# Performance work log

Hardware: AMD Instinct MI355X
Metric: run time of the kernel (lower is better)

## Reference

```python
import jax, jax.numpy as jnp
import numpy as np

N_NODES = 50000
N_EDGES = 800000
D_IN = 128
D_OUT = 128


def setup_inputs() -> dict:
    key = jax.random.key(0)
    ks = jax.random.split(key, 6)
    x = jax.random.normal(ks[0], (N_NODES, D_IN), dtype=jnp.float32)
    edge_src = jax.random.randint(ks[1], (N_EDGES,), 0, N_NODES)
    edge_dst = jax.random.randint(ks[2], (N_EDGES,), 0, N_NODES)
    edge_val = jax.random.uniform(ks[3], (N_EDGES,), dtype=jnp.float32)
    W = jax.random.normal(ks[4], (D_OUT, D_IN), dtype=jnp.float32) / np.sqrt(D_IN)
    b = jax.random.normal(ks[5], (D_OUT,), dtype=jnp.float32) * 0.01
    return {"x": x, "edge_src": edge_src, "edge_dst": edge_dst,
            "edge_val": edge_val, "W": W, "b": b}


def reference(x, edge_src, edge_dst, edge_val, W, b):
    # h = sparse.mm(adj, x): for each edge (dst, src, val): h[dst] += val * x[src]
    msgs = edge_val[:, None] * x[edge_src]            # [E, D_IN]
    h = jax.ops.segment_sum(msgs, edge_dst, num_segments=N_NODES)  # [N, D_IN]
    # nn.Linear: h @ W.T + b, then relu activation
    out = jnp.einsum('nd,od->no', h, W) + b           # [N, D_OUT]
    return jax.nn.relu(out)
```

## Files before the change

kernel.cpp:

```cpp
#include <hip/hip_runtime.h>
#include <hip/hip_bf16.h>

#define N_NODES 50000
#define N_EDGES 800000
#define D 128
#define CAP 64
#define EPT 8
#define BUCKET_NB 391
#define GEMM_NB 256
#define AGG_BPQ 782
#define YSLICE (N_NODES * 16)

static_assert(N_NODES < 65536, "src must fit in 16 bits for epack");
static_assert(BUCKET_NB * 256 * EPT >= N_EDGES, "bucket grid covers all edges");

typedef __attribute__((ext_vector_type(8))) short short8;
typedef __attribute__((ext_vector_type(4))) float f32x4;
typedef unsigned int uint;
typedef unsigned short ushort;

__device__ __forceinline__ ushort f2bf(float f) {
    uint u = __float_as_uint(f);
    u += 0x7fffu + ((u >> 16) & 1u);
    return (ushort)(u >> 16);
}

__device__ __forceinline__ float bflo(uint u) { return __uint_as_float(u << 16); }
__device__ __forceinline__ float bfhi(uint u) { return __uint_as_float(u & 0xffff0000u); }


__global__ __launch_bounds__(256) void sgcn_fat(
    const float* __restrict__ x, const float* __restrict__ W,
    const int* __restrict__ src, const int* __restrict__ dst,
    const float* __restrict__ val, int* __restrict__ deg,
    uint* __restrict__ epack, ushort* __restrict__ y)
{
    if (blockIdx.x < BUCKET_NB) {
        int t = blockIdx.x * 256 + threadIdx.x;
        const int T = BUCKET_NB * 256;
        int  d[EPT], s[EPT], r[EPT];
        float v[EPT];
        bool ok[EPT];
#pragma unroll
        for (int i = 0; i < EPT; ++i) {
            int e = t + i * T;
            ok[i] = e < N_EDGES;
            if (ok[i]) { d[i] = dst[e]; s[i] = src[e]; v[i] = val[e]; }
        }
#pragma unroll
        for (int i = 0; i < EPT; ++i)
            if (ok[i]) r[i] = atomicAdd(&deg[d[i]], 1);
#pragma unroll
        for (int i = 0; i < EPT; ++i)
            if (ok[i] && r[i] < CAP)
                epack[(size_t)d[i] * CAP + r[i]] = ((uint)f2bf(v[i]) << 16) | (uint)s[i];
        return;
    }

    int gb   = blockIdx.x - BUCKET_NB;
    int wave = threadIdx.x >> 6;
    int lane = threadIdx.x & 63;
    int lm = lane & 15;
    int kb = lane >> 4;

    short8 bfr[8][4];
#pragma unroll
    for (int nt = 0; nt < 8; ++nt)
#pragma unroll
        for (int kk = 0; kk < 4; ++kk) {
            const float* wp = W + (nt * 16 + lm) * D + kk * 32 + kb * 8;
            float4 a = *reinterpret_cast<const float4*>(wp);
            float4 c = *reinterpret_cast<const float4*>(wp + 4);
            short8 s;
            s[0] = (short)f2bf(a.x); s[1] = (short)f2bf(a.y);
            s[2] = (short)f2bf(a.z); s[3] = (short)f2bf(a.w);
            s[4] = (short)f2bf(c.x); s[5] = (short)f2bf(c.y);
            s[6] = (short)f2bf(c.z); s[7] = (short)f2bf(c.w);
            bfr[nt][kk] = s;
        }

    const int nMT = N_NODES / 16;
    int mt0 = gb * 4 + wave;
    const int strideMT = GEMM_NB * 4;
    for (int mt = mt0; mt < nMT; mt += strideMT) {
        int m0 = mt * 16;
        const float* xrow = x + (long)(m0 + lm) * D + kb * 8;
        short8 afr[4];
#pragma unroll
        for (int kk = 0; kk < 4; ++kk) {
            float4 a = *reinterpret_cast<const float4*>(xrow + kk * 32);
            float4 c = *reinterpret_cast<const float4*>(xrow + kk * 32 + 4);
            short8 s;
            s[0] = (short)f2bf(a.x); s[1] = (short)f2bf(a.y);
            s[2] = (short)f2bf(a.z); s[3] = (short)f2bf(a.w);
            s[4] = (short)f2bf(c.x); s[5] = (short)f2bf(c.y);
            s[6] = (short)f2bf(c.z); s[7] = (short)f2bf(c.w);
            afr[kk] = s;
        }
#pragma unroll
        for (int nt = 0; nt < 8; ++nt) {
            f32x4 acc = {0.f, 0.f, 0.f, 0.f};
#pragma unroll
            for (int kk = 0; kk < 4; ++kk)
                acc = __builtin_amdgcn_mfma_f32_16x16x32_bf16(afr[kk], bfr[nt][kk], acc, 0, 0, 0);
            int q = nt >> 1;
            ushort* yp = y + ((size_t)q * N_NODES + (m0 + kb * 4)) * 32 + (nt & 1) * 16 + lm;
#pragma unroll
            for (int r = 0; r < 4; ++r)
                yp[(size_t)r * 32] = f2bf(acc[r]);
        }
    }
}


__global__ __launch_bounds__(256) void sgcn_aggregate(
    const uint* __restrict__ yb, const int* __restrict__ deg,
    const uint* __restrict__ ep, const float* __restrict__ bias,
    float* __restrict__ out)
{
    int q  = blockIdx.x & 3;
    int nb = blockIdx.x >> 2;
    int n  = nb * 64 + (threadIdx.x >> 2);
    if (n >= N_NODES) return;
    int c4 = threadIdx.x & 3;
    int ch = q * 32 + c4 * 8;
    const uint* ys = yb + (size_t)q * YSLICE;

    float4 bv0 = *reinterpret_cast<const float4*>(bias + ch);
    float4 bv1 = *reinterpret_cast<const float4*>(bias + ch + 4);

    int dn = deg[n]; if (dn > CAP) dn = CAP;
    int j0 = n * CAP, j1 = j0 + dn;
    float a0 = 0.f, a1 = 0.f, a2 = 0.f, a3 = 0.f;
    float a4 = 0.f, a5 = 0.f, a6 = 0.f, a7 = 0.f;
    int j = j0;
    for (; j + 2 <= j1; j += 2) {
        uint p0 = ep[j];
        uint p1 = ep[j + 1];
        uint4 u0 = *reinterpret_cast<const uint4*>(ys + (size_t)(p0 & 0xffffu) * 16 + c4 * 4);
        uint4 u1 = *reinterpret_cast<const uint4*>(ys + (size_t)(p1 & 0xffffu) * 16 + c4 * 4);
        float v0 = __uint_as_float(p0 & 0xffff0000u);
        float v1 = __uint_as_float(p1 & 0xffff0000u);
        a0 += v0 * bflo(u0.x) + v1 * bflo(u1.x);
        a1 += v0 * bfhi(u0.x) + v1 * bfhi(u1.x);
        a2 += v0 * bflo(u0.y) + v1 * bflo(u1.y);
        a3 += v0 * bfhi(u0.y) + v1 * bfhi(u1.y);
        a4 += v0 * bflo(u0.z) + v1 * bflo(u1.z);
        a5 += v0 * bfhi(u0.z) + v1 * bfhi(u1.z);
        a6 += v0 * bflo(u0.w) + v1 * bflo(u1.w);
        a7 += v0 * bfhi(u0.w) + v1 * bfhi(u1.w);
    }
    if (j < j1) {
        uint p = ep[j];
        uint4 u = *reinterpret_cast<const uint4*>(ys + (size_t)(p & 0xffffu) * 16 + c4 * 4);
        float v = __uint_as_float(p & 0xffff0000u);
        a0 += v * bflo(u.x); a1 += v * bfhi(u.x);
        a2 += v * bflo(u.y); a3 += v * bfhi(u.y);
        a4 += v * bflo(u.z); a5 += v * bfhi(u.z);
        a6 += v * bflo(u.w); a7 += v * bfhi(u.w);
    }
    f32x4 r0, r1;
    r0[0] = fmaxf(a0 + bv0.x, 0.f);
    r0[1] = fmaxf(a1 + bv0.y, 0.f);
    r0[2] = fmaxf(a2 + bv0.z, 0.f);
    r0[3] = fmaxf(a3 + bv0.w, 0.f);
    r1[0] = fmaxf(a4 + bv1.x, 0.f);
    r1[1] = fmaxf(a5 + bv1.y, 0.f);
    r1[2] = fmaxf(a6 + bv1.z, 0.f);
    r1[3] = fmaxf(a7 + bv1.w, 0.f);
    f32x4* op = reinterpret_cast<f32x4*>(out + (long)n * D + ch);
    __builtin_nontemporal_store(r0, op);
    __builtin_nontemporal_store(r1, op + 1);
}

extern "C" void kernel_launch(void* const* d_in, const int* in_sizes, int n_in,
                              void* d_out, int out_size, void* d_ws, size_t ws_size,
                              hipStream_t stream) {
    const float* x   = (const float*)d_in[0];
    const int*   es  = (const int*)d_in[1];
    const int*   ed  = (const int*)d_in[2];
    const float* ev  = (const float*)d_in[3];
    const float* W   = (const float*)d_in[4];
    const float* b   = (const float*)d_in[5];
    float* out = (float*)d_out;

    char* ws = (char*)d_ws;
    size_t off = 0;
    uint* yb    = (uint*)(ws + off); off += (size_t)4 * YSLICE * sizeof(uint);
    uint* epack = (uint*)(ws + off); off += (size_t)N_NODES * CAP * sizeof(uint);
    int*  deg   = (int*) (ws + off); off += (size_t)N_NODES * sizeof(int);

    (void)hipMemsetAsync(deg, 0, (size_t)N_NODES * sizeof(int), stream);
    sgcn_fat<<<BUCKET_NB + GEMM_NB, 256, 0, stream>>>(x, W, es, ed, ev, deg, epack, (ushort*)yb);
    sgcn_aggregate<<<AGG_BPQ * 4, 256, 0, stream>>>(yb, deg, epack, b, out);
}
```

Measured before the change: 100.7 us.

## Split edge bucketing by destination half to overlap with aggregation

Bucketing is split into two passes by destination node range. The second-half bucketing runs in the same launch as aggregation of the first half, and a third kernel aggregates the second half. The aim is to hide atomic bucketing cost behind the GEMM and aggregation work. In exchange the edge dst array is read twice, the src/val loads become filtered, and there is one more kernel launch.

```diff
diff --git a/kernel.cpp b/kernel.cpp
--- a/kernel.cpp
+++ b/kernel.cpp
@@ -2,13 +2,14 @@
 #include <hip/hip_bf16.h>
 
 #define N_NODES 50000
+#define HALF 25000
 #define N_EDGES 800000
 #define D 128
 #define CAP 64
 #define EPT 8
 #define BUCKET_NB 391
 #define GEMM_NB 256
-#define AGG_BPQ 782
+#define AGG_HB 391
 #define YSLICE (N_NODES * 16)
 
 static_assert(N_NODES < 65536, "src must fit in 16 bits for epack");
@@ -29,99 +30,45 @@
 __device__ __forceinline__ float bfhi(uint u) { return __uint_as_float(u & 0xffff0000u); }
 
 
-__global__ __launch_bounds__(256) void sgcn_fat(
-    const float* __restrict__ x, const float* __restrict__ W,
-    const int* __restrict__ src, const int* __restrict__ dst,
+__device__ __forceinline__ void bucket_body(
+    int bid, const int* __restrict__ src, const int* __restrict__ dst,
     const float* __restrict__ val, int* __restrict__ deg,
-    uint* __restrict__ epack, ushort* __restrict__ y)
-{
-    if (blockIdx.x < BUCKET_NB) {
-        int t = blockIdx.x * 256 + threadIdx.x;
-        const int T = BUCKET_NB * 256;
-        int  d[EPT], s[EPT], r[EPT];
-        float v[EPT];
-        bool ok[EPT];
-#pragma unroll
-        for (int i = 0; i < EPT; ++i) {
-            int e = t + i * T;
-            ok[i] = e < N_EDGES;
-            if (ok[i]) { d[i] = dst[e]; s[i] = src[e]; v[i] = val[e]; }
-        }
-#pragma unroll
-        for (int i = 0; i < EPT; ++i)
-            if (ok[i]) r[i] = atomicAdd(&deg[d[i]], 1);
-#pragma unroll
-        for (int i = 0; i < EPT; ++i)
-            if (ok[i] && r[i] < CAP)
-                epack[(size_t)d[i] * CAP + r[i]] = ((uint)f2bf(v[i]) << 16) | (uint)s[i];
-        return;
-    }
-
-    int gb   = blockIdx.x - BUCKET_NB;
-    int wave = threadIdx.x >> 6;
-    int lane = threadIdx.x & 63;
-    int lm = lane & 15;
-    int kb = lane >> 4;
-
-    short8 bfr[8][4];
-#pragma unroll
-    for (int nt = 0; nt < 8; ++nt)
-#pragma unroll
-        for (int kk = 0; kk < 4; ++kk) {
-            const float* wp = W + (nt * 16 + lm) * D + kk * 32 + kb * 8;
-            float4 a = *reinterpret_cast<const float4*>(wp);
-            float4 c = *reinterpret_cast<const float4*>(wp + 4);
-            short8 s;
-            s[0] = (short)f2bf(a.x); s[1] = (short)f2bf(a.y);
-            s[2] = (short)f2bf(a.z); s[3] = (short)f2bf(a.w);
-            s[4] = (short)f2bf(c.x); s[5] = (short)f2bf(c.y);
-            s[6] = (short)f2bf(c.z); s[7] = (short)f2bf(c.w);
-            bfr[nt][kk] = s;
-        }
-
-    const int nMT = N_NODES / 16;
-    int mt0 = gb * 4 + wave;
-    const int strideMT = GEMM_NB * 4;
-    for (int mt = mt0; mt < nMT; mt += strideMT) {
-        int m0 = mt * 16;
-        const float* xrow = x + (long)(m0 + lm) * D + kb * 8;
-        short8 afr[4];
-#pragma unroll
-        for (int kk = 0; kk < 4; ++kk) {
-            float4 a = *reinterpret_cast<const float4*>(xrow + kk * 32);
-            float4 c = *reinterpret_cast<const float4*>(xrow + kk * 32 + 4);
-            short8 s;
-            s[0] = (short)f2bf(a.x); s[1] = (short)f2bf(a.y);
-            s[2] = (short)f2bf(a.z); s[3] = (short)f2bf(a.w);
-            s[4] = (short)f2bf(c.x); s[5] = (short)f2bf(c.y);
-            s[6] = (short)f2bf(c.z); s[7] = (short)f2bf(c.w);
-            afr[kk] = s;
-        }
-#pragma unroll
-        for (int nt = 0; nt < 8; ++nt) {
-            f32x4 acc = {0.f, 0.f, 0.f, 0.f};
-#pragma unroll
-            for (int kk = 0; kk < 4; ++kk)
-                acc = __builtin_amdgcn_mfma_f32_16x16x32_bf16(afr[kk], bfr[nt][kk], acc, 0, 0, 0);
-            int q = nt >> 1;
-            ushort* yp = y + ((size_t)q * N_NODES + (m0 + kb * 4)) * 32 + (nt & 1) * 16 + lm;
-#pragma unroll
-            for (int r = 0; r < 4; ++r)
-                yp[(size_t)r * 32] = f2bf(acc[r]);
-        }
-    }
-}
-
-
-__global__ __launch_bounds__(256) void sgcn_aggregate(
-    const uint* __restrict__ yb, const int* __restrict__ deg,
+    uint* __restrict__ epack, int dlo, int dhi)
+{
+    int t = bid * 256 + threadIdx.x;
+    const int T = BUCKET_NB * 256;
+    int  d[EPT], s[EPT], r[EPT];
+    float v[EPT];
+    bool ok[EPT];
+#pragma unroll
+    for (int i = 0; i < EPT; ++i) {
+        int e = t + i * T;
+        ok[i] = false;
+        if (e < N_EDGES) {
+            d[i] = dst[e];
+            ok[i] = (d[i] >= dlo) && (d[i] < dhi);
+            if (ok[i]) { s[i] = src[e]; v[i] = val[e]; }
+        }
+    }
+#pragma unroll
+    for (int i = 0; i < EPT; ++i)
+        if (ok[i]) r[i] = atomicAdd(&deg[d[i]], 1);
+#pragma unroll
+    for (int i = 0; i < EPT; ++i)
+        if (ok[i] && r[i] < CAP)
+            epack[(size_t)d[i] * CAP + r[i]] = ((uint)f2bf(v[i]) << 16) | (uint)s[i];
+}
+
+__device__ __forceinline__ void agg_body(
+    int bid, int nbase, const uint* __restrict__ yb, const int* __restrict__ deg,
     const uint* __restrict__ ep, const float* __restrict__ bias,
     float* __restrict__ out)
 {
-    int q  = blockIdx.x & 3;
-    int nb = blockIdx.x >> 2;
-    int n  = nb * 64 + (threadIdx.x >> 2);
-    if (n >= N_NODES) return;
+    int q  = bid & 3;
+    int nb = bid >> 2;
+    int ln = nb * 64 + (threadIdx.x >> 2);
+    if (ln >= HALF) return;
+    int n  = nbase + ln;
     int c4 = threadIdx.x & 3;
     int ch = q * 32 + c4 * 8;
     const uint* ys = yb + (size_t)q * YSLICE;
@@ -173,6 +120,96 @@
     __builtin_nontemporal_store(r1, op + 1);
 }
 
+
+__global__ __launch_bounds__(256) void sgcn_p1(
+    const float* __restrict__ x, const float* __restrict__ W,
+    const int* __restrict__ src, const int* __restrict__ dst,
+    const float* __restrict__ val, int* __restrict__ deg,
+    uint* __restrict__ epack, ushort* __restrict__ y)
+{
+    if (blockIdx.x < BUCKET_NB) {
+        bucket_body(blockIdx.x, src, dst, val, deg, epack, 0, HALF);
+        return;
+    }
+
+    int gb   = blockIdx.x - BUCKET_NB;
+    int wave = threadIdx.x >> 6;
+    int lane = threadIdx.x & 63;
+    int lm = lane & 15;
+    int kb = lane >> 4;
+
+    short8 bfr[8][4];
+#pragma unroll
+    for (int nt = 0; nt < 8; ++nt)
+#pragma unroll
+        for (int kk = 0; kk < 4; ++kk) {
+            const float* wp = W + (nt * 16 + lm) * D + kk * 32 + kb * 8;
+            float4 a = *reinterpret_cast<const float4*>(wp);
+            float4 c = *reinterpret_cast<const float4*>(wp + 4);
+            short8 s;
+            s[0] = (short)f2bf(a.x); s[1] = (short)f2bf(a.y);
+            s[2] = (short)f2bf(a.z); s[3] = (short)f2bf(a.w);
+            s[4] = (short)f2bf(c.x); s[5] = (short)f2bf(c.y);
+            s[6] = (short)f2bf(c.z); s[7] = (short)f2bf(c.w);
+            bfr[nt][kk] = s;
+        }
+
+    const int nMT = N_NODES / 16;
+    int mt0 = gb * 4 + wave;
+    const int strideMT = GEMM_NB * 4;
+    for (int mt = mt0; mt < nMT; mt += strideMT) {
+        int m0 = mt * 16;
+        const float* xrow = x + (long)(m0 + lm) * D + kb * 8;
+        short8 afr[4];
+#pragma unroll
+        for (int kk = 0; kk < 4; ++kk) {
+            float4 a = *reinterpret_cast<const float4*>(xrow + kk * 32);
+            float4 c = *reinterpret_cast<const float4*>(xrow + kk * 32 + 4);
+            short8 s;
+            s[0] = (short)f2bf(a.x); s[1] = (short)f2bf(a.y);
+            s[2] = (short)f2bf(a.z); s[3] = (short)f2bf(a.w);
+            s[4] = (short)f2bf(c.x); s[5] = (short)f2bf(c.y);
+            s[6] = (short)f2bf(c.z); s[7] = (short)f2bf(c.w);
+            afr[kk] = s;
+        }
+#pragma unroll
+        for (int nt = 0; nt < 8; ++nt) {
+            f32x4 acc = {0.f, 0.f, 0.f, 0.f};
+#pragma unroll
+            for (int kk = 0; kk < 4; ++kk)
+                acc = __builtin_amdgcn_mfma_f32_16x16x32_bf16(afr[kk], bfr[nt][kk], acc, 0, 0, 0);
+            int q = nt >> 1;
+            ushort* yp = y + ((size_t)q * N_NODES + (m0 + kb * 4)) * 32 + (nt & 1) * 16 + lm;
+#pragma unroll
+            for (int r = 0; r < 4; ++r)
+                yp[(size_t)r * 32] = f2bf(acc[r]);
+        }
+    }
+}
+
+
+__global__ __launch_bounds__(256) void sgcn_p2(
+    const int* __restrict__ src, const int* __restrict__ dst,
+    const float* __restrict__ val, int* __restrict__ deg,
+    uint* __restrict__ epack, const uint* __restrict__ yb,
+    const float* __restrict__ bias, float* __restrict__ out)
+{
+    if (blockIdx.x < BUCKET_NB) {
+        bucket_body(blockIdx.x, src, dst, val, deg, epack, HALF, N_NODES);
+        return;
+    }
+    agg_body(blockIdx.x - BUCKET_NB, 0, yb, deg, epack, bias, out);
+}
+
+
+__global__ __launch_bounds__(256) void sgcn_p3(
+    const uint* __restrict__ yb, const int* __restrict__ deg,
+    const uint* __restrict__ ep, const float* __restrict__ bias,
+    float* __restrict__ out)
+{
+    agg_body(blockIdx.x, HALF, yb, deg, ep, bias, out);
+}
+
 extern "C" void kernel_launch(void* const* d_in, const int* in_sizes, int n_in,
                               void* d_out, int out_size, void* d_ws, size_t ws_size,
                               hipStream_t stream) {
@@ -191,6 +228,7 @@
     int*  deg   = (int*) (ws + off); off += (size_t)N_NODES * sizeof(int);
 
     (void)hipMemsetAsync(deg, 0, (size_t)N_NODES * sizeof(int), stream);
-    sgcn_fat<<<BUCKET_NB + GEMM_NB, 256, 0, stream>>>(x, W, es, ed, ev, deg, epack, (ushort*)yb);
-    sgcn_aggregate<<<AGG_BPQ * 4, 256, 0, stream>>>(yb, deg, epack, b, out);
-}
+    sgcn_p1<<<BUCKET_NB + GEMM_NB, 256, 0, stream>>>(x, W, es, ed, ev, deg, epack, (ushort*)yb);
+    sgcn_p2<<<BUCKET_NB + AGG_HB * 4, 256, 0, stream>>>(es, ed, ev, deg, epack, yb, b, out);
+    sgcn_p3<<<AGG_HB * 4, 256, 0, stream>>>(yb, deg, epack, b, out);
+}
```

After: 117.5 us. 16.7% more time.
